# Kernel tuning notes

Hardware: AMD Instinct MI355X
Metric: run time of the kernel (lower is better)

Reference implementation:

```python
import jax, jax.numpy as jnp
import numpy as np
import math

B, S, D, H, WIDTH, NHW = 8, 1024, 512, 8, 8, 2
DK = D // H
S2 = S + 2 * WIDTH


def setup_inputs() -> dict:
    key = jax.random.key(0)
    ks = jax.random.split(key, 12)
    sc = 1.0 / math.sqrt(D)
    return {
        "x": jax.random.normal(ks[0], (B, S, D), jnp.float32),
        "l_attn_W": jax.random.normal(ks[1], (4, D, D), jnp.float32) * sc,  # q,k,v,out
        "l_attn_b": jnp.zeros((4, D), jnp.float32),
        "r_attn_W": jax.random.normal(ks[2], (4, D, D), jnp.float32) * sc,
        "r_attn_b": jnp.zeros((4, D), jnp.float32),
        "left_pad": jax.random.normal(ks[3], (WIDTH, D), jnp.float32) * sc,
        "right_pad": jax.random.normal(ks[4], (WIDTH, D), jnp.float32) * sc,
        "left_w": jax.random.normal(ks[5], (WIDTH + 1,), jnp.float32),
        "right_w": jax.random.normal(ks[6], (WIDTH + 1,), jnp.float32),
        "l_hw_W": jax.random.normal(ks[7], (NHW, D, 2 * D), jnp.float32) * sc,
        "l_hw_b": jnp.zeros((NHW, 2 * D), jnp.float32),
        "r_hw_W": jax.random.normal(ks[8], (NHW, D, 2 * D), jnp.float32) * sc,
        "r_hw_b": jnp.zeros((NHW, 2 * D), jnp.float32),
    }


def _mha(x, W, b, mask):
    # x: [B, S2, D]; W: [4, D, D]; mask: [1, S2, S2] bool (True = keep)
    q = (x @ W[0] + b[0]).reshape(B, S2, H, DK)
    k = (x @ W[1] + b[1]).reshape(B, S2, H, DK)
    v = (x @ W[2] + b[2]).reshape(B, S2, H, DK)
    scores = jnp.einsum('bihd,bjhd->bhij', q, k) / math.sqrt(DK)
    scores = jnp.where(mask[:, None], scores, jnp.float32(-1e9))
    p = jax.nn.softmax(scores, axis=-1)
    o = jnp.einsum('bhij,bjhd->bihd', p, v).reshape(B, S2, D)
    return o @ W[3] + b[3]


def _highway(x, Ws, bs):
    # AllenNLP-style Highway: projected -> [nonlinear | gate]
    for i in range(NHW):
        proj = x @ Ws[i] + bs[i]
        nl = jax.nn.relu(proj[..., :D])
        g = jax.nn.sigmoid(proj[..., D:])
        x = g * x + (1.0 - g) * nl
    return x


def reference(x, l_attn_W, l_attn_b, r_attn_W, r_attn_b, left_pad, right_pad,
              left_w, right_w, l_hw_W, l_hw_b, r_hw_W, r_hw_b):
    new_in = jnp.concatenate([
        jnp.broadcast_to(left_pad, (B, WIDTH, D)), x,
        jnp.broadcast_to(right_pad, (B, WIDTH, D))], axis=1)  # [B, S2, D]
    idx = jnp.arange(S2)
    diff = idx[:, None] - idx[None, :]
    lmask = ((diff >= 0) & (diff <= WIDTH + 1))[None]          # attend to [i-width-1, i]
    rmask = ((diff <= 0) & (diff >= -(WIDTH + 1)))[None]       # attend to [i, i+width+1]
    nl_attn = _mha(new_in, l_attn_W, l_attn_b, lmask)
    nr_attn = _mha(new_in, r_attn_W, r_attn_b, rmask)
    left_out = nl_attn[:, WIDTH:WIDTH + S, :]   # position end = start + width
    right_out = nr_attn[:, WIDTH:WIDTH + S, :]
    # relative-position weighted sliding windows (vectorized over all steps)
    lrel = sum(left_w[j] * new_in[:, j:j + S, :] for j in range(WIDTH + 1))
    rrel = sum(right_w[j] * new_in[:, WIDTH + j:WIDTH + j + S, :] for j in range(WIDTH + 1))
    left_out = _highway(left_out + lrel, l_hw_W, l_hw_b)
    right_out = _highway(right_out + rrel, r_hw_W, r_hw_b)
    out = jnp.concatenate([left_out, right_out], axis=-1)  # [B, S, 2D]
    return out[None]  # [1, B, S, 2D] matching torch stack layout
```

## Files before the change

kernel.cpp:

```cpp
#include <hip/hip_runtime.h>


#define B_ 8
#define S_ 1024
#define D_ 512
#define H_ 8
#define DK_ 64
#define WIDTH_ 8
#define S2_ 1040
#define NHW_ 2

typedef short bf16x8 __attribute__((ext_vector_type(8)));
typedef float f32x4 __attribute__((ext_vector_type(4)));

__device__ __forceinline__ float us2f(unsigned short u) {
  union { unsigned int i; float f; } c; c.i = ((unsigned int)u) << 16; return c.f;
}
__device__ __forceinline__ unsigned short f2us(float f) {
  union { float f; unsigned int i; } c; c.f = f;
  unsigned int x = c.i;
  return (unsigned short)((x + 0x7fffu + ((x >> 16) & 1u)) >> 16);
}
__device__ __forceinline__ unsigned int pack2(float a, float b) {
  return (unsigned int)f2us(a) | ((unsigned int)f2us(b) << 16);
}
__device__ __forceinline__ void async16(const void* g, void* l) {
  __builtin_amdgcn_global_load_lds(
      (const __attribute__((address_space(1))) void*)g,
      (__attribute__((address_space(3))) void*)l, 16, 0, 0);
}
__device__ __forceinline__ void unpack8(uint4 u, float* f) {
  unsigned int w[4] = {u.x, u.y, u.z, u.w};
  #pragma unroll
  for (int c = 0; c < 4; ++c) {
    union { unsigned int i; float g; } lo, hi;
    lo.i = w[c] << 16;
    hi.i = w[c] & 0xffff0000u;
    f[2 * c] = lo.g;
    f[2 * c + 1] = hi.g;
  }
}

__global__ __launch_bounds__(256) void k_prep(
    const float* __restrict__ x,
    const float* __restrict__ lpad, const float* __restrict__ rpad,
    const float* __restrict__ lW, const float* __restrict__ rW,
    const float* __restrict__ lb, const float* __restrict__ rb,
    const float* __restrict__ lhwW, const float* __restrict__ rhwW,
    unsigned short* __restrict__ WTall, unsigned short* __restrict__ WTp,
    unsigned short* __restrict__ hWT,
    unsigned short* __restrict__ nin, float* __restrict__ qkvbias)
{
  __shared__ float tile[32][33];
  const size_t DD = (size_t)D_ * D_;
  int bx = blockIdx.x;
  int tx = threadIdx.x & 31, ty = threadIdx.x >> 5;

  if (bx < 2048) {
    int sl = bx >> 8, rem = bx & 255;
    int side = sl >> 2, slice = sl & 3;
    int c0 = (rem & 15) * 32, r0 = (rem >> 4) * 32;
    const float* src = (side ? rW : lW) + (size_t)slice * DD;
    unsigned short* dst = (slice < 3) ? WTall + (size_t)(side * 3 + slice) * DD
                                      : WTp + (size_t)side * DD;
    #pragma unroll
    for (int i = 0; i < 4; ++i)
      tile[ty + i * 8][tx] = src[(size_t)(r0 + ty + i * 8) * D_ + c0 + tx];
    __syncthreads();
    #pragma unroll
    for (int i = 0; i < 4; ++i)
      dst[(size_t)(c0 + ty + i * 8) * D_ + r0 + tx] = f2us(tile[tx][ty + i * 8]);
    return;
  }
  if (bx < 4096) {
    int idx = bx - 2048;
    int sl = idx >> 9, rem = idx & 511;
    int c0 = (rem & 31) * 32, r0 = (rem >> 5) * 32;
    const float* src = ((sl >> 1) ? rhwW : lhwW) + (size_t)(sl & 1) * 512 * 1024;
    unsigned short* dst = hWT + (size_t)sl * 1024 * 512;
    #pragma unroll
    for (int i = 0; i < 4; ++i)
      tile[ty + i * 8][tx] = src[(size_t)(r0 + ty + i * 8) * 1024 + c0 + tx];
    __syncthreads();
    #pragma unroll
    for (int i = 0; i < 4; ++i) {
      int c = c0 + ty + i * 8;
      int cm = c & 511;
      int j = cm >> 4;
      int jl = j & 7;
      int Bq = ((jl >> 2) << 3) + (jl & 3) + ((c >= 512) ? 4 : 0);
      int q = (j >> 3) * 256 + Bq * 16 + (cm & 15);
      dst[(size_t)q * 512 + r0 + tx] = f2us(tile[tx][ty + i * 8]);
    }
    return;
  }
  int gid = (bx - 4096) * 256 + threadIdx.x;
  const int NTH = B_ * S2_ * 64;
  if (gid >= NTH) {
    int t = gid - NTH;
    if (t < 1536) qkvbias[t] = lb[t];
    else if (t < 3072) qkvbias[t] = rb[t - 1536];
    return;
  }
  int c8 = (gid & 63) << 3;
  int row = gid >> 6;
  int b = row / S2_;
  int t = row - b * S2_;
  const float* src;
  if (t < WIDTH_)            src = lpad + (size_t)t * D_ + c8;
  else if (t >= S_ + WIDTH_) src = rpad + (size_t)(t - S_ - WIDTH_) * D_ + c8;
  else                       src = x + ((size_t)b * S_ + (t - WIDTH_)) * D_ + c8;
  float4 a = *reinterpret_cast<const float4*>(src);
  float4 c = *reinterpret_cast<const float4*>(src + 4);
  uint4 o;
  o.x = pack2(a.x, a.y); o.y = pack2(a.z, a.w);
  o.z = pack2(c.x, c.y); o.w = pack2(c.z, c.w);
  *reinterpret_cast<uint4*>(nin + (size_t)row * D_ + c8) = o;
}

__global__ __launch_bounds__(256) void k_gemm_mfma(
    const unsigned short* __restrict__ A,
    const unsigned short* __restrict__ BT,
    const float* __restrict__ bias,
    unsigned short* __restrict__ C,
    int M, int N, int K)
{
  __shared__ unsigned short As[128 * 64];
  __shared__ unsigned short Bs[128 * 64];

  const int tid = threadIdx.x;
  const int w = tid >> 6;
  const int l = tid & 63;

  const int gx = gridDim.x;
  const int nwg = gx * gridDim.y;
  const int flat = blockIdx.y * gx + blockIdx.x;
  const int cpx = nwg >> 3;
  const int nf = (flat & 7) * cpx + (flat >> 3);
  const int bm = (nf / gx) * 128;
  const int bn = (nf % gx) * 128;

  const int wrow = (w >> 1) * 64;
  const int wcol = (w & 1) * 64;

  const int lr = l >> 3;
  const int sk = (((l & 7) ^ lr) & 7) * 8;
  const unsigned short* Ap = A + (size_t)(bm + w * 8 + lr) * K + sk;
  const unsigned short* Bp = BT + (size_t)(bn + w * 8 + lr) * K + sk;
  unsigned short* lA = &As[w * 512];
  unsigned short* lB = &Bs[w * 512];
  const size_t K32 = (size_t)32 * K;

  const int fl = l & 15;
  const int fq = l >> 4;
  const int fx = fl & 7;

  f32x4 acc[4][4];
  #pragma unroll
  for (int mi = 0; mi < 4; ++mi)
    #pragma unroll
    for (int ni = 0; ni < 4; ++ni) acc[mi][ni] = (f32x4){0.f, 0.f, 0.f, 0.f};

  for (int k0 = 0; k0 < K; k0 += 64) {
    #pragma unroll
    for (int r = 0; r < 4; ++r) {
      async16(Ap + k0 + r * K32, lA + r * 2048);
      async16(Bp + k0 + r * K32, lB + r * 2048);
    }
    __syncthreads();
    #pragma unroll
    for (int s = 0; s < 2; ++s) {
      bf16x8 af[4], bfr[4];
      #pragma unroll
      for (int mi = 0; mi < 4; ++mi)
        af[mi] = *reinterpret_cast<const bf16x8*>(
            &As[(wrow + mi * 16 + fl) * 64 + (((s * 4 + fq) ^ fx) * 8)]);
      #pragma unroll
      for (int ni = 0; ni < 4; ++ni)
        bfr[ni] = *reinterpret_cast<const bf16x8*>(
            &Bs[(wcol + ni * 16 + fl) * 64 + (((s * 4 + fq) ^ fx) * 8)]);
      #pragma unroll
      for (int mi = 0; mi < 4; ++mi)
        #pragma unroll
        for (int ni = 0; ni < 4; ++ni)
          acc[mi][ni] = __builtin_amdgcn_mfma_f32_16x16x32_bf16(
              af[mi], bfr[ni], acc[mi][ni], 0, 0, 0);
    }
    __syncthreads();
  }

  float bv[4];
  #pragma unroll
  for (int ni = 0; ni < 4; ++ni) bv[ni] = bias[bn + wcol + ni * 16 + fl];

  const int rbase = (l >> 4) * 4;
  #pragma unroll
  for (int mi = 0; mi < 4; ++mi) {
    #pragma unroll
    for (int r = 0; r < 4; ++r) {
      int row = bm + wrow + mi * 16 + rbase + r;
      unsigned short* Cp = C + (size_t)row * N + bn + wcol + fl;
      #pragma unroll
      for (int ni = 0; ni < 4; ++ni)
        Cp[ni * 16] = f2us(acc[mi][ni][r] + bv[ni]);
    }
  }
}

template <int EPI>
__global__ __launch_bounds__(512, 2) void k_gemm256(
    const unsigned short* __restrict__ Abase, size_t aStrZ,
    const unsigned short* __restrict__ BTbase, size_t bStrZ,
    const float* __restrict__ bias0, const float* __restrict__ bias1,
    unsigned short* __restrict__ Cbf, float* __restrict__ Cfp,
    int M, int N)
{
  __shared__ __align__(16) unsigned short smem[65536];
  const int tid = threadIdx.x;
  const int w = tid >> 6, l = tid & 63;
  const int wm = w >> 2, wn = w & 3;
  const int fl = l & 15, fq = l >> 4;
  const int z = blockIdx.z;
  const unsigned short* A = Abase + (size_t)z * aStrZ;
  const unsigned short* BT = BTbase + (size_t)z * bStrZ;
  const int bm = blockIdx.y * 256, bn = blockIdx.x * 256;

  const int xorb = (fl & 7) << 4;
  const int cs0 = ((fq * 16) ^ xorb) >> 1;
  const int cs1 = ((64 + fq * 16) ^ xorb) >> 1;

  const int rr = l >> 3;
  const int ce = (((l & 7) * 16) ^ (rr << 4)) >> 1;
  const unsigned short* gA[2][2];
  const unsigned short* gB[2][2];
  #pragma unroll
  for (int i = 0; i < 2; ++i)
    #pragma unroll
    for (int h = 0; h < 2; ++h) {
      int ra = bm + h * 128 + (2 * w + i) * 8 + rr;
      if (ra > M - 1) ra = M - 1;
      gA[i][h] = A + (size_t)ra * 512 + ce;
      int rb = bn + h * 128 + (2 * w + i) * 8 + rr;
      gB[i][h] = BT + (size_t)rb * 512 + ce;
    }

  f32x4 acc[8][4];
  #pragma unroll
  for (int mi = 0; mi < 8; ++mi)
    #pragma unroll
    for (int ni = 0; ni < 4; ++ni) acc[mi][ni] = (f32x4){0.f, 0.f, 0.f, 0.f};

  bf16x8 ar[4][2], br[2][2];

#define BAR() __builtin_amdgcn_s_barrier()
#define STGA(buf, h, kt) do { \
    async16(gA[0][h] + (kt) * 64, &smem[((buf) * 2 + (h)) * 8192 + (2 * w) * 512]); \
    async16(gA[1][h] + (kt) * 64, &smem[((buf) * 2 + (h)) * 8192 + (2 * w + 1) * 512]); } while (0)
#define STGB(buf, h, kt) do { \
    async16(gB[0][h] + (kt) * 64, &smem[32768 + ((buf) * 2 + (h)) * 8192 + (2 * w) * 512]); \
    async16(gB[1][h] + (kt) * 64, &smem[32768 + ((buf) * 2 + (h)) * 8192 + (2 * w + 1) * 512]); } while (0)
#define LDA(buf, h) do { const unsigned short* p_ = &smem[((buf) * 2 + (h)) * 8192]; \
    _Pragma("unroll") for (int m4 = 0; m4 < 4; ++m4) { \
      int ro_ = ((2 * m4 + wm) * 16 + fl) * 64; \
      ar[m4][0] = *reinterpret_cast<const bf16x8*>(p_ + ro_ + cs0); \
      ar[m4][1] = *reinterpret_cast<const bf16x8*>(p_ + ro_ + cs1); } } while (0)
#define LDB(buf, h) do { const unsigned short* p_ = &smem[32768 + ((buf) * 2 + (h)) * 8192]; \
    _Pragma("unroll") for (int n2 = 0; n2 < 2; ++n2) { \
      int ro_ = ((4 * n2 + wn) * 16 + fl) * 64; \
      br[n2][0] = *reinterpret_cast<const bf16x8*>(p_ + ro_ + cs0); \
      br[n2][1] = *reinterpret_cast<const bf16x8*>(p_ + ro_ + cs1); } } while (0)
#define QUAD(miH, niH) do { __builtin_amdgcn_s_setprio(1); \
    _Pragma("unroll") for (int m4 = 0; m4 < 4; ++m4) \
      _Pragma("unroll") for (int n2 = 0; n2 < 2; ++n2) \
        _Pragma("unroll") for (int s_ = 0; s_ < 2; ++s_) \
          acc[(miH) * 4 + m4][(niH) * 2 + n2] = __builtin_amdgcn_mfma_f32_16x16x32_bf16( \
              ar[m4][s_], br[n2][s_], acc[(miH) * 4 + m4][(niH) * 2 + n2], 0, 0, 0); \
    __builtin_amdgcn_s_setprio(0); } while (0)

  STGA(0, 0, 0); STGB(0, 0, 0); STGB(0, 1, 0); STGA(0, 1, 0);
  STGA(1, 0, 1); STGB(1, 1, 1); STGA(1, 1, 1);
  asm volatile("s_waitcnt vmcnt(6)" ::: "memory");
  BAR();

  #pragma unroll 1
  for (int it = 0; it < 4; ++it) {
    const int t1 = 2 * it + 1, t2 = 2 * it + 2, t3 = 2 * it + 3;
    LDA(0, 0); LDB(0, 0);
    STGB(1, 0, t1);
    BAR(); QUAD(0, 0); BAR();
    LDB(0, 1);
    if (t2 < 8) STGA(0, 0, t2);
    BAR(); QUAD(0, 1); BAR();
    LDA(0, 1);
    if (t2 < 8) STGB(0, 1, t2);
    BAR(); QUAD(1, 1); BAR();
    LDB(0, 0);
    if (t2 < 8) STGA(0, 1, t2);
    BAR(); QUAD(1, 0);
    if (it < 3) asm volatile("s_waitcnt vmcnt(6)" ::: "memory");
    else        asm volatile("s_waitcnt vmcnt(0)" ::: "memory");
    BAR();
    LDA(1, 0); LDB(1, 0);
    if (t2 < 8) STGB(0, 0, t2);
    BAR(); QUAD(0, 0); BAR();
    LDB(1, 1);
    if (t3 < 8) STGA(1, 0, t3);
    BAR(); QUAD(0, 1); BAR();
    LDA(1, 1);
    if (t3 < 8) STGB(1, 1, t3);
    BAR(); QUAD(1, 1); BAR();
    LDB(1, 0);
    if (t3 < 8) STGA(1, 1, t3);
    BAR(); QUAD(1, 0);
    asm volatile("s_waitcnt vmcnt(6)" ::: "memory");
    BAR();
  }
#undef BAR
#undef STGA
#undef STGB
#undef LDA
#undef LDB
#undef QUAD

  {
    const float* bias = z ? bias1 : bias0;
    const size_t MS = (size_t)B_ * S_ * D_;
    float bnl[2], bg[2]; int xs[2];
    #pragma unroll
    for (int np = 0; np < 2; ++np) {
      xs[np] = (blockIdx.x * 8 + np * 4 + wn) * 16 + fl;
      bnl[np] = bias[xs[np]];
      bg[np]  = bias[512 + xs[np]];
    }
    #pragma unroll
    for (int mi = 0; mi < 8; ++mi) {
      #pragma unroll
      for (int r = 0; r < 4; ++r) {
        int gr = bm + (2 * mi + wm) * 16 + fq * 4 + r;
        #pragma unroll
        for (int np = 0; np < 2; ++np) {
          float nl = fmaxf(acc[mi][2 * np][r] + bnl[np], 0.f);
          float g  = 1.f / (1.f + __expf(-(acc[mi][2 * np + 1][r] + bg[np])));
          float xv = us2f(A[(size_t)gr * 512 + xs[np]]);
          float res = g * xv + (1.f - g) * nl;
          if (EPI == 2) Cfp[(size_t)gr * 1024 + (size_t)z * 512 + xs[np]] = res;
          else Cbf[(size_t)z * MS + (size_t)gr * 512 + xs[np]] = f2us(res);
        }
      }
    }
  }
}

__global__ __launch_bounds__(256) void k_gemm_proj(
    const unsigned short* __restrict__ ctx,
    const unsigned short* __restrict__ WTp,
    const unsigned short* __restrict__ nin,
    const float* __restrict__ lb3, const float* __restrict__ rb3,
    const float* __restrict__ wrel0, const float* __restrict__ wrel1,
    unsigned short* __restrict__ hwx)
{
  __shared__ unsigned short smem[128 * 136];
  unsigned short* As = smem;
  unsigned short* Bs = smem + 8192;
  const int K = 512, N = 512;
  const size_t MS = (size_t)B_ * S_ * D_;

  const int z = blockIdx.z;
  const unsigned short* A = ctx + (size_t)z * MS;
  const unsigned short* BT = WTp + (size_t)z * 512 * 512;
  const float* bias = z ? rb3 : lb3;
  const float* wrel = z ? wrel1 : wrel0;
  const int off = z * WIDTH_;

  const int tid = threadIdx.x;
  const int w = tid >> 6;
  const int l = tid & 63;
  const int bm = blockIdx.y * 128;
  const int bn = blockIdx.x * 128;
  const int wrow = (w >> 1) * 64;
  const int wcol = (w & 1) * 64;

  const int lr = l >> 3;
  const int sk = (((l & 7) ^ lr) & 7) * 8;
  const unsigned short* Ap = A + (size_t)(bm + w * 8 + lr) * K + sk;
  const unsigned short* Bp = BT + (size_t)(bn + w * 8 + lr) * K + sk;
  unsigned short* lA = &As[w * 512];
  unsigned short* lB = &Bs[w * 512];
  const size_t K32 = (size_t)32 * K;

  const int fl = l & 15;
  const int fq = l >> 4;
  const int fx = fl & 7;

  f32x4 acc[4][4];
  #pragma unroll
  for (int mi = 0; mi < 4; ++mi)
    #pragma unroll
    for (int ni = 0; ni < 4; ++ni) acc[mi][ni] = (f32x4){0.f, 0.f, 0.f, 0.f};

  for (int k0 = 0; k0 < K; k0 += 64) {
    #pragma unroll
    for (int r = 0; r < 4; ++r) {
      async16(Ap + k0 + r * K32, lA + r * 2048);
      async16(Bp + k0 + r * K32, lB + r * 2048);
    }
    __syncthreads();
    #pragma unroll
    for (int s = 0; s < 2; ++s) {
      bf16x8 af[4], bfr[4];
      #pragma unroll
      for (int mi = 0; mi < 4; ++mi)
        af[mi] = *reinterpret_cast<const bf16x8*>(
            &As[(wrow + mi * 16 + fl) * 64 + (((s * 4 + fq) ^ fx) * 8)]);
      #pragma unroll
      for (int ni = 0; ni < 4; ++ni)
        bfr[ni] = *reinterpret_cast<const bf16x8*>(
            &Bs[(wcol + ni * 16 + fl) * 64 + (((s * 4 + fq) ^ fx) * 8)]);
      #pragma unroll
      for (int mi = 0; mi < 4; ++mi)
        #pragma unroll
        for (int ni = 0; ni < 4; ++ni)
          acc[mi][ni] = __builtin_amdgcn_mfma_f32_16x16x32_bf16(
              af[mi], bfr[ni], acc[mi][ni], 0, 0, 0);
    }
    __syncthreads();
  }

  float bv[4];
  #pragma unroll
  for (int ni = 0; ni < 4; ++ni) bv[ni] = bias[bn + wcol + ni * 16 + fl];
  const int rbase = (l >> 4) * 4;
  #pragma unroll
  for (int mi = 0; mi < 4; ++mi)
    #pragma unroll
    for (int r = 0; r < 4; ++r)
      #pragma unroll
      for (int ni = 0; ni < 4; ++ni)
        smem[(wrow + mi * 16 + rbase + r) * 136 + wcol + ni * 16 + fl] =
            f2us(acc[mi][ni][r] + bv[ni]);
  __syncthreads();

  const int trow = tid >> 4;
  const int tcol = (tid & 15) * 8;
  const float w0 = wrel[0], w1 = wrel[1], w2 = wrel[2], w3 = wrel[3],
              w4 = wrel[4], w5 = wrel[5], w6 = wrel[6], w7 = wrel[7],
              w8 = wrel[8];
  const float wj[9] = {w0, w1, w2, w3, w4, w5, w6, w7, w8};
  #pragma unroll
  for (int i = 0; i < 8; ++i) {
    int r = trow + i * 16;
    int gr = bm + r;
    int b = gr >> 10, s = gr & (S_ - 1);
    float a8[8];
    unpack8(*reinterpret_cast<const uint4*>(&smem[r * 136 + tcol]), a8);
    const unsigned short* np =
        nin + ((size_t)b * S2_ + off + s) * D_ + bn + tcol;
    #pragma unroll
    for (int j = 0; j < 9; ++j) {
      float nf[8];
      unpack8(*reinterpret_cast<const uint4*>(np + (size_t)j * D_), nf);
      #pragma unroll
      for (int e = 0; e < 8; ++e) a8[e] += wj[j] * nf[e];
    }
    uint4 o;
    o.x = pack2(a8[0], a8[1]); o.y = pack2(a8[2], a8[3]);
    o.z = pack2(a8[4], a8[5]); o.w = pack2(a8[6], a8[7]);
    *reinterpret_cast<uint4*>(
        hwx + (size_t)z * MS + (size_t)gr * D_ + bn + tcol) = o;
  }
}

__global__ __launch_bounds__(256) void k_attn_window(
    const unsigned short* __restrict__ qkv,
    unsigned short* __restrict__ ctx)
{
  int wid = (blockIdx.x * 256 + threadIdx.x) >> 6;
  int lane = threadIdx.x & 63;
  int sg = wid & 255;
  int b = (wid >> 8) & 7;
  int dir = wid >> 11;
  int s0 = sg << 2;
  int i0 = s0 + WIDTH_;

  const size_t base = (size_t)b * S2_ * 3072 + dir * 1536;
  const int c0 = lane * 8;

  float qf[4][8];
  #pragma unroll
  for (int r = 0; r < 4; ++r)
    unpack8(*reinterpret_cast<const uint4*>(
        qkv + base + (size_t)(i0 + r) * 3072 + c0), qf[r]);

  float sc[4][10];
  float mx[4] = {-1e30f, -1e30f, -1e30f, -1e30f};
  #pragma unroll
  for (int t = 0; t < 13; ++t) {
    int j = (dir == 0) ? (i0 - 9 + t) : (i0 + t);
    bool ok = (j >= 0 && j < S2_);
    float kf[8];
    if (ok)
      unpack8(*reinterpret_cast<const uint4*>(
          qkv + base + (size_t)j * 3072 + 512 + c0), kf);
    #pragma unroll
    for (int r = 0; r < 4; ++r) {
      if (t < r || t > r + 9) continue;
      float sv = -1e30f;
      if (ok) {
        float p = qf[r][0] * kf[0];
        #pragma unroll
        for (int e = 1; e < 8; ++e) p += qf[r][e] * kf[e];
        p += __shfl_xor(p, 1);
        p += __shfl_xor(p, 2);
        p += __shfl_xor(p, 4);
        sv = p * 0.125f;
      }
      sc[r][t - r] = sv;
      mx[r] = fmaxf(mx[r], sv);
    }
  }

  float inv[4];
  #pragma unroll
  for (int r = 0; r < 4; ++r) {
    float den = 0.f;
    #pragma unroll
    for (int u = 0; u < 10; ++u) {
      sc[r][u] = (sc[r][u] > -1e29f) ? __expf(sc[r][u] - mx[r]) : 0.f;
      den += sc[r][u];
    }
    inv[r] = 1.f / den;
  }

  float acc[4][8];
  #pragma unroll
  for (int r = 0; r < 4; ++r)
    #pragma unroll
    for (int e = 0; e < 8; ++e) acc[r][e] = 0.f;

  #pragma unroll
  for (int t = 0; t < 13; ++t) {
    int j = (dir == 0) ? (i0 - 9 + t) : (i0 + t);
    bool ok = (j >= 0 && j < S2_);
    float vf[8];
    if (ok)
      unpack8(*reinterpret_cast<const uint4*>(
          qkv + base + (size_t)j * 3072 + 1024 + c0), vf);
    #pragma unroll
    for (int r = 0; r < 4; ++r) {
      if (t < r || t > r + 9) continue;
      if (ok) {
        float p = sc[r][t - r];
        #pragma unroll
        for (int e = 0; e < 8; ++e) acc[r][e] += p * vf[e];
      }
    }
  }

  #pragma unroll
  for (int r = 0; r < 4; ++r) {
    uint4 o;
    o.x = pack2(acc[r][0] * inv[r], acc[r][1] * inv[r]);
    o.y = pack2(acc[r][2] * inv[r], acc[r][3] * inv[r]);
    o.z = pack2(acc[r][4] * inv[r], acc[r][5] * inv[r]);
    o.w = pack2(acc[r][6] * inv[r], acc[r][7] * inv[r]);
    *reinterpret_cast<uint4*>(
        ctx + (((size_t)dir * B_ + b) * S_ + s0 + r) * D_ + c0) = o;
  }
}

extern "C" void kernel_launch(void* const* d_in, const int* in_sizes, int n_in,
                              void* d_out, int out_size, void* d_ws, size_t ws_size,
                              hipStream_t stream) {
  const float* x    = (const float*)d_in[0];
  const float* lW   = (const float*)d_in[1];
  const float* lb   = (const float*)d_in[2];
  const float* rW   = (const float*)d_in[3];
  const float* rb   = (const float*)d_in[4];
  const float* lpad = (const float*)d_in[5];
  const float* rpad = (const float*)d_in[6];
  const float* lw   = (const float*)d_in[7];
  const float* rw   = (const float*)d_in[8];
  const float* lhwW = (const float*)d_in[9];
  const float* lhwb = (const float*)d_in[10];
  const float* rhwW = (const float*)d_in[11];
  const float* rhwb = (const float*)d_in[12];
  float* out = (float*)d_out;
  unsigned short* ws = (unsigned short*)d_ws;

  const size_t NIN  = (size_t)B_ * S2_ * D_;
  const size_t NQKV = (size_t)B_ * S2_ * 3072;
  const size_t MS   = (size_t)B_ * S_ * D_;
  const size_t DD   = (size_t)D_ * D_;
  const size_t LHW  = (size_t)1024 * 512;

  unsigned short* nin   = ws;
  unsigned short* qkv   = nin + NIN;
  unsigned short* ctx   = qkv + NQKV;
  unsigned short* hwx   = ctx + 2 * MS;
  unsigned short* hwy   = hwx + 2 * MS;
  unsigned short* WTall = hwy + 2 * MS;
  unsigned short* WTp   = WTall + 6 * DD;
  unsigned short* hWT   = WTp + 2 * DD;
  float* qkvbias        = (float*)(hWT + 4 * LHW);

  k_prep<<<6188, 256, 0, stream>>>(x, lpad, rpad, lW, rW, lb, rb, lhwW, rhwW,
                                   WTall, WTp, hWT, nin, qkvbias);

  const int MQ = B_ * S2_;

  {
    dim3 g(3072 / 128, MQ / 128, 1);
    k_gemm_mfma<<<g, 256, 0, stream>>>(nin, WTall, qkvbias, qkv, MQ, 3072, D_);
  }

  k_attn_window<<<(2 * B_ * S_) / 16, 256, 0, stream>>>(qkv, ctx);

  {
    dim3 g(D_ / 128, (B_ * S_) / 128, 2);
    k_gemm_proj<<<g, 256, 0, stream>>>(ctx, WTp, nin, lb + 3 * D_, rb + 3 * D_,
                                       lw, rw, hwx);
  }

  {
    dim3 g(1024 / 256, (B_ * S_) / 256, 2);
    k_gemm256<1><<<g, 512, 0, stream>>>(hwx, MS, hWT, 2 * LHW,
                                        lhwb, rhwb, hwy, nullptr,
                                        B_ * S_, 1024);
    k_gemm256<2><<<g, 512, 0, stream>>>(hwy, MS, hWT + LHW, 2 * LHW,
                                        lhwb + 1024, rhwb + 1024,
                                        nullptr, out, B_ * S_, 1024);
  }
}
```

Measured before the change: 236.4 us.

## Fuse attention, projection and highway layers into one cooperative persistent kernel

Replaces four separate launches (window attention, output projection, two highway GEMMs) with a single cooperative kernel of 256 blocks that runs each stage in turn and separates them with grid-wide syncs. Each block processes one attention slice, then two 128-tile projection GEMMs, then one 256-tile highway GEMM per layer. This aims to remove launch gaps and tail effects between kernels. In exchange, grid syncs add overhead, the grid is fixed at 256 blocks of 512 threads, and the 128KB shared buffer limits residency, so the attention and projection stages may run with less parallelism than before.

```diff
diff --git a/kernel.cpp b/kernel.cpp
--- a/kernel.cpp
+++ b/kernel.cpp
@@ -1,4 +1,6 @@
 #include <hip/hip_runtime.h>
+#include <hip/hip_cooperative_groups.h>
+namespace cg = cooperative_groups;
 
 
 #define B_ 8
@@ -207,23 +209,20 @@
   }
 }
 
-template <int EPI>
-__global__ __launch_bounds__(512, 2) void k_gemm256(
-    const unsigned short* __restrict__ Abase, size_t aStrZ,
-    const unsigned short* __restrict__ BTbase, size_t bStrZ,
-    const float* __restrict__ bias0, const float* __restrict__ bias1,
-    unsigned short* __restrict__ Cbf, float* __restrict__ Cfp,
-    int M, int N)
+__device__ __forceinline__ void hw_layer(
+    unsigned short* smem,
+    const unsigned short* __restrict__ A,
+    const unsigned short* __restrict__ BT,
+    const float* __restrict__ bias,
+    unsigned short* __restrict__ Obf,
+    float* __restrict__ Ofp,
+    int bx, int by, bool final_)
 {
-  __shared__ __align__(16) unsigned short smem[65536];
   const int tid = threadIdx.x;
   const int w = tid >> 6, l = tid & 63;
   const int wm = w >> 2, wn = w & 3;
   const int fl = l & 15, fq = l >> 4;
-  const int z = blockIdx.z;
-  const unsigned short* A = Abase + (size_t)z * aStrZ;
-  const unsigned short* BT = BTbase + (size_t)z * bStrZ;
-  const int bm = blockIdx.y * 256, bn = blockIdx.x * 256;
+  const int bm = by * 256, bn = bx * 256;
 
   const int xorb = (fl & 7) << 4;
   const int cs0 = ((fq * 16) ^ xorb) >> 1;
@@ -238,7 +237,6 @@
     #pragma unroll
     for (int h = 0; h < 2; ++h) {
       int ra = bm + h * 128 + (2 * w + i) * 8 + rr;
-      if (ra > M - 1) ra = M - 1;
       gA[i][h] = A + (size_t)ra * 512 + ce;
       int rb = bn + h * 128 + (2 * w + i) * 8 + rr;
       gB[i][h] = BT + (size_t)rb * 512 + ce;
@@ -322,249 +320,275 @@
 #undef LDB
 #undef QUAD
 
-  {
-    const float* bias = z ? bias1 : bias0;
-    const size_t MS = (size_t)B_ * S_ * D_;
-    float bnl[2], bg[2]; int xs[2];
-    #pragma unroll
-    for (int np = 0; np < 2; ++np) {
-      xs[np] = (blockIdx.x * 8 + np * 4 + wn) * 16 + fl;
-      bnl[np] = bias[xs[np]];
-      bg[np]  = bias[512 + xs[np]];
-    }
-    #pragma unroll
-    for (int mi = 0; mi < 8; ++mi) {
-      #pragma unroll
-      for (int r = 0; r < 4; ++r) {
-        int gr = bm + (2 * mi + wm) * 16 + fq * 4 + r;
-        #pragma unroll
-        for (int np = 0; np < 2; ++np) {
-          float nl = fmaxf(acc[mi][2 * np][r] + bnl[np], 0.f);
-          float g  = 1.f / (1.f + __expf(-(acc[mi][2 * np + 1][r] + bg[np])));
-          float xv = us2f(A[(size_t)gr * 512 + xs[np]]);
-          float res = g * xv + (1.f - g) * nl;
-          if (EPI == 2) Cfp[(size_t)gr * 1024 + (size_t)z * 512 + xs[np]] = res;
-          else Cbf[(size_t)z * MS + (size_t)gr * 512 + xs[np]] = f2us(res);
-        }
-      }
-    }
-  }
-}
-
-__global__ __launch_bounds__(256) void k_gemm_proj(
-    const unsigned short* __restrict__ ctx,
+  float bnl[2], bg[2]; int xs[2];
+  #pragma unroll
+  for (int np = 0; np < 2; ++np) {
+    xs[np] = (bx * 8 + np * 4 + wn) * 16 + fl;
+    bnl[np] = bias[xs[np]];
+    bg[np]  = bias[512 + xs[np]];
+  }
+  #pragma unroll
+  for (int mi = 0; mi < 8; ++mi) {
+    #pragma unroll
+    for (int r = 0; r < 4; ++r) {
+      int gr = bm + (2 * mi + wm) * 16 + fq * 4 + r;
+      #pragma unroll
+      for (int np = 0; np < 2; ++np) {
+        float nl = fmaxf(acc[mi][2 * np][r] + bnl[np], 0.f);
+        float g  = 1.f / (1.f + __expf(-(acc[mi][2 * np + 1][r] + bg[np])));
+        float xv = us2f(A[(size_t)gr * 512 + xs[np]]);
+        float res = g * xv + (1.f - g) * nl;
+        if (final_) Ofp[(size_t)gr * 1024 + xs[np]] = res;
+        else        Obf[(size_t)gr * 512 + xs[np]] = f2us(res);
+      }
+    }
+  }
+}
+
+__global__ __launch_bounds__(512, 2) void k_mega(
+    const unsigned short* __restrict__ qkv,
+    unsigned short* __restrict__ ctx,
     const unsigned short* __restrict__ WTp,
     const unsigned short* __restrict__ nin,
     const float* __restrict__ lb3, const float* __restrict__ rb3,
     const float* __restrict__ wrel0, const float* __restrict__ wrel1,
-    unsigned short* __restrict__ hwx)
+    unsigned short* __restrict__ hwx,
+    unsigned short* __restrict__ hwy,
+    const unsigned short* __restrict__ hWT,
+    const float* __restrict__ lhwb, const float* __restrict__ rhwb,
+    float* __restrict__ out)
 {
-  __shared__ unsigned short smem[128 * 136];
-  unsigned short* As = smem;
-  unsigned short* Bs = smem + 8192;
-  const int K = 512, N = 512;
+  __shared__ __align__(16) unsigned short smem[65536];
+  cg::grid_group grid = cg::this_grid();
   const size_t MS = (size_t)B_ * S_ * D_;
-
-  const int z = blockIdx.z;
-  const unsigned short* A = ctx + (size_t)z * MS;
-  const unsigned short* BT = WTp + (size_t)z * 512 * 512;
-  const float* bias = z ? rb3 : lb3;
-  const float* wrel = z ? wrel1 : wrel0;
-  const int off = z * WIDTH_;
-
-  const int tid = threadIdx.x;
-  const int w = tid >> 6;
-  const int l = tid & 63;
-  const int bm = blockIdx.y * 128;
-  const int bn = blockIdx.x * 128;
-  const int wrow = (w >> 1) * 64;
-  const int wcol = (w & 1) * 64;
-
-  const int lr = l >> 3;
-  const int sk = (((l & 7) ^ lr) & 7) * 8;
-  const unsigned short* Ap = A + (size_t)(bm + w * 8 + lr) * K + sk;
-  const unsigned short* Bp = BT + (size_t)(bn + w * 8 + lr) * K + sk;
-  unsigned short* lA = &As[w * 512];
-  unsigned short* lB = &Bs[w * 512];
-  const size_t K32 = (size_t)32 * K;
-
-  const int fl = l & 15;
-  const int fq = l >> 4;
-  const int fx = fl & 7;
-
-  f32x4 acc[4][4];
-  #pragma unroll
-  for (int mi = 0; mi < 4; ++mi)
-    #pragma unroll
-    for (int ni = 0; ni < 4; ++ni) acc[mi][ni] = (f32x4){0.f, 0.f, 0.f, 0.f};
-
-  for (int k0 = 0; k0 < K; k0 += 64) {
-    #pragma unroll
-    for (int r = 0; r < 4; ++r) {
-      async16(Ap + k0 + r * K32, lA + r * 2048);
-      async16(Bp + k0 + r * K32, lB + r * 2048);
-    }
+  const size_t LHW = (size_t)1024 * 512;
+
+  {
+    const int lane = threadIdx.x & 63;
+    const int wv = blockIdx.x * 8 + (threadIdx.x >> 6);
+    const int c0 = lane * 8;
+    const int sg = wv & 255;
+    const int b = (wv >> 8) & 7;
+    const int s0 = sg << 2;
+    const int i0 = s0 + WIDTH_;
+
+    #pragma unroll 1
+    for (int dir = 0; dir < 2; ++dir) {
+      const size_t base = (size_t)b * S2_ * 3072 + dir * 1536;
+
+      float qf[4][8];
+      #pragma unroll
+      for (int r = 0; r < 4; ++r)
+        unpack8(*reinterpret_cast<const uint4*>(
+            qkv + base + (size_t)(i0 + r) * 3072 + c0), qf[r]);
+
+      float sc[4][10];
+      float mx[4] = {-1e30f, -1e30f, -1e30f, -1e30f};
+      #pragma unroll
+      for (int t = 0; t < 13; ++t) {
+        int j = (dir == 0) ? (i0 - 9 + t) : (i0 + t);
+        bool ok = (j >= 0 && j < S2_);
+        float kf[8];
+        if (ok)
+          unpack8(*reinterpret_cast<const uint4*>(
+              qkv + base + (size_t)j * 3072 + 512 + c0), kf);
+        #pragma unroll
+        for (int r = 0; r < 4; ++r) {
+          if (t < r || t > r + 9) continue;
+          float sv = -1e30f;
+          if (ok) {
+            float p = qf[r][0] * kf[0];
+            #pragma unroll
+            for (int e = 1; e < 8; ++e) p += qf[r][e] * kf[e];
+            p += __shfl_xor(p, 1);
+            p += __shfl_xor(p, 2);
+            p += __shfl_xor(p, 4);
+            sv = p * 0.125f;
+          }
+          sc[r][t - r] = sv;
+          mx[r] = fmaxf(mx[r], sv);
+        }
+      }
+
+      float inv[4];
+      #pragma unroll
+      for (int r = 0; r < 4; ++r) {
+        float den = 0.f;
+        #pragma unroll
+        for (int u = 0; u < 10; ++u) {
+          sc[r][u] = (sc[r][u] > -1e29f) ? __expf(sc[r][u] - mx[r]) : 0.f;
+          den += sc[r][u];
+        }
+        inv[r] = 1.f / den;
+      }
+
+      float acc[4][8];
+      #pragma unroll
+      for (int r = 0; r < 4; ++r)
+        #pragma unroll
+        for (int e = 0; e < 8; ++e) acc[r][e] = 0.f;
+
+      #pragma unroll
+      for (int t = 0; t < 13; ++t) {
+        int j = (dir == 0) ? (i0 - 9 + t) : (i0 + t);
+        bool ok = (j >= 0 && j < S2_);
+        float vf[8];
+        if (ok)
+          unpack8(*reinterpret_cast<const uint4*>(
+              qkv + base + (size_t)j * 3072 + 1024 + c0), vf);
+        #pragma unroll
+        for (int r = 0; r < 4; ++r) {
+          if (t < r || t > r + 9) continue;
+          if (ok) {
+            float p = sc[r][t - r];
+            #pragma unroll
+            for (int e = 0; e < 8; ++e) acc[r][e] += p * vf[e];
+          }
+        }
+      }
+
+      #pragma unroll
+      for (int r = 0; r < 4; ++r) {
+        uint4 o;
+        o.x = pack2(acc[r][0] * inv[r], acc[r][1] * inv[r]);
+        o.y = pack2(acc[r][2] * inv[r], acc[r][3] * inv[r]);
+        o.z = pack2(acc[r][4] * inv[r], acc[r][5] * inv[r]);
+        o.w = pack2(acc[r][6] * inv[r], acc[r][7] * inv[r]);
+        *reinterpret_cast<uint4*>(
+            ctx + (((size_t)dir * B_ + b) * S_ + s0 + r) * D_ + c0) = o;
+      }
+    }
+  }
+  __threadfence();
+  grid.sync();
+
+  {
+    const int h = threadIdx.x >> 8;
+    const int t2 = threadIdx.x & 255;
+    const int v = blockIdx.x * 2 + h;
+    const int bx = v & 3, by = (v >> 2) & 63, z = v >> 8;
+    unsigned short* sm = smem + h * 17408;
+    unsigned short* As = sm;
+    unsigned short* Bs = sm + 8192;
+    const int K = 512;
+    const unsigned short* A = ctx + (size_t)z * MS;
+    const unsigned short* BT = WTp + (size_t)z * 262144;
+    const float* bias = z ? rb3 : lb3;
+    const float* wrel = z ? wrel1 : wrel0;
+    const int off = z * WIDTH_;
+
+    const int w = t2 >> 6;
+    const int l = t2 & 63;
+    const int bm = by * 128;
+    const int bn = bx * 128;
+    const int wrow = (w >> 1) * 64;
+    const int wcol = (w & 1) * 64;
+
+    const int lr = l >> 3;
+    const int sk = (((l & 7) ^ lr) & 7) * 8;
+    const unsigned short* Ap = A + (size_t)(bm + w * 8 + lr) * K + sk;
+    const unsigned short* Bp = BT + (size_t)(bn + w * 8 + lr) * K + sk;
+    unsigned short* lA = &As[w * 512];
+    unsigned short* lB = &Bs[w * 512];
+    const size_t K32 = (size_t)32 * K;
+
+    const int fl = l & 15;
+    const int fq = l >> 4;
+    const int fx = fl & 7;
+
+    f32x4 acc[4][4];
+    #pragma unroll
+    for (int mi = 0; mi < 4; ++mi)
+      #pragma unroll
+      for (int ni = 0; ni < 4; ++ni) acc[mi][ni] = (f32x4){0.f, 0.f, 0.f, 0.f};
+
+    for (int k0 = 0; k0 < K; k0 += 64) {
+      #pragma unroll
+      for (int r = 0; r < 4; ++r) {
+        async16(Ap + k0 + r * K32, lA + r * 2048);
+        async16(Bp + k0 + r * K32, lB + r * 2048);
+      }
+      __syncthreads();
+      #pragma unroll
+      for (int s = 0; s < 2; ++s) {
+        bf16x8 af[4], bfr[4];
+        #pragma unroll
+        for (int mi = 0; mi < 4; ++mi)
+          af[mi] = *reinterpret_cast<const bf16x8*>(
+              &As[(wrow + mi * 16 + fl) * 64 + (((s * 4 + fq) ^ fx) * 8)]);
+        #pragma unroll
+        for (int ni = 0; ni < 4; ++ni)
+          bfr[ni] = *reinterpret_cast<const bf16x8*>(
+              &Bs[(wcol + ni * 16 + fl) * 64 + (((s * 4 + fq) ^ fx) * 8)]);
+        #pragma unroll
+        for (int mi = 0; mi < 4; ++mi)
+          #pragma unroll
+          for (int ni = 0; ni < 4; ++ni)
+            acc[mi][ni] = __builtin_amdgcn_mfma_f32_16x16x32_bf16(
+                af[mi], bfr[ni], acc[mi][ni], 0, 0, 0);
+      }
+      __syncthreads();
+    }
+
+    float bv[4];
+    #pragma unroll
+    for (int ni = 0; ni < 4; ++ni) bv[ni] = bias[bn + wcol + ni * 16 + fl];
+    const int rbase = (l >> 4) * 4;
+    #pragma unroll
+    for (int mi = 0; mi < 4; ++mi)
+      #pragma unroll
+      for (int r = 0; r < 4; ++r)
+        #pragma unroll
+        for (int ni = 0; ni < 4; ++ni)
+          sm[(wrow + mi * 16 + rbase + r) * 136 + wcol + ni * 16 + fl] =
+              f2us(acc[mi][ni][r] + bv[ni]);
     __syncthreads();
-    #pragma unroll
-    for (int s = 0; s < 2; ++s) {
-      bf16x8 af[4], bfr[4];
-      #pragma unroll
-      for (int mi = 0; mi < 4; ++mi)
-        af[mi] = *reinterpret_cast<const bf16x8*>(
-            &As[(wrow + mi * 16 + fl) * 64 + (((s * 4 + fq) ^ fx) * 8)]);
-      #pragma unroll
-      for (int ni = 0; ni < 4; ++ni)
-        bfr[ni] = *reinterpret_cast<const bf16x8*>(
-            &Bs[(wcol + ni * 16 + fl) * 64 + (((s * 4 + fq) ^ fx) * 8)]);
-      #pragma unroll
-      for (int mi = 0; mi < 4; ++mi)
-        #pragma unroll
-        for (int ni = 0; ni < 4; ++ni)
-          acc[mi][ni] = __builtin_amdgcn_mfma_f32_16x16x32_bf16(
-              af[mi], bfr[ni], acc[mi][ni], 0, 0, 0);
-    }
-    __syncthreads();
-  }
-
-  float bv[4];
-  #pragma unroll
-  for (int ni = 0; ni < 4; ++ni) bv[ni] = bias[bn + wcol + ni * 16 + fl];
-  const int rbase = (l >> 4) * 4;
-  #pragma unroll
-  for (int mi = 0; mi < 4; ++mi)
-    #pragma unroll
-    for (int r = 0; r < 4; ++r)
-      #pragma unroll
-      for (int ni = 0; ni < 4; ++ni)
-        smem[(wrow + mi * 16 + rbase + r) * 136 + wcol + ni * 16 + fl] =
-            f2us(acc[mi][ni][r] + bv[ni]);
-  __syncthreads();
-
-  const int trow = tid >> 4;
-  const int tcol = (tid & 15) * 8;
-  const float w0 = wrel[0], w1 = wrel[1], w2 = wrel[2], w3 = wrel[3],
-              w4 = wrel[4], w5 = wrel[5], w6 = wrel[6], w7 = wrel[7],
-              w8 = wrel[8];
-  const float wj[9] = {w0, w1, w2, w3, w4, w5, w6, w7, w8};
-  #pragma unroll
-  for (int i = 0; i < 8; ++i) {
-    int r = trow + i * 16;
-    int gr = bm + r;
-    int b = gr >> 10, s = gr & (S_ - 1);
-    float a8[8];
-    unpack8(*reinterpret_cast<const uint4*>(&smem[r * 136 + tcol]), a8);
-    const unsigned short* np =
-        nin + ((size_t)b * S2_ + off + s) * D_ + bn + tcol;
-    #pragma unroll
-    for (int j = 0; j < 9; ++j) {
-      float nf[8];
-      unpack8(*reinterpret_cast<const uint4*>(np + (size_t)j * D_), nf);
-      #pragma unroll
-      for (int e = 0; e < 8; ++e) a8[e] += wj[j] * nf[e];
-    }
-    uint4 o;
-    o.x = pack2(a8[0], a8[1]); o.y = pack2(a8[2], a8[3]);
-    o.z = pack2(a8[4], a8[5]); o.w = pack2(a8[6], a8[7]);
-    *reinterpret_cast<uint4*>(
-        hwx + (size_t)z * MS + (size_t)gr * D_ + bn + tcol) = o;
-  }
-}
-
-__global__ __launch_bounds__(256) void k_attn_window(
-    const unsigned short* __restrict__ qkv,
-    unsigned short* __restrict__ ctx)
-{
-  int wid = (blockIdx.x * 256 + threadIdx.x) >> 6;
-  int lane = threadIdx.x & 63;
-  int sg = wid & 255;
-  int b = (wid >> 8) & 7;
-  int dir = wid >> 11;
-  int s0 = sg << 2;
-  int i0 = s0 + WIDTH_;
-
-  const size_t base = (size_t)b * S2_ * 3072 + dir * 1536;
-  const int c0 = lane * 8;
-
-  float qf[4][8];
-  #pragma unroll
-  for (int r = 0; r < 4; ++r)
-    unpack8(*reinterpret_cast<const uint4*>(
-        qkv + base + (size_t)(i0 + r) * 3072 + c0), qf[r]);
-
-  float sc[4][10];
-  float mx[4] = {-1e30f, -1e30f, -1e30f, -1e30f};
-  #pragma unroll
-  for (int t = 0; t < 13; ++t) {
-    int j = (dir == 0) ? (i0 - 9 + t) : (i0 + t);
-    bool ok = (j >= 0 && j < S2_);
-    float kf[8];
-    if (ok)
-      unpack8(*reinterpret_cast<const uint4*>(
-          qkv + base + (size_t)j * 3072 + 512 + c0), kf);
-    #pragma unroll
-    for (int r = 0; r < 4; ++r) {
-      if (t < r || t > r + 9) continue;
-      float sv = -1e30f;
-      if (ok) {
-        float p = qf[r][0] * kf[0];
-        #pragma unroll
-        for (int e = 1; e < 8; ++e) p += qf[r][e] * kf[e];
-        p += __shfl_xor(p, 1);
-        p += __shfl_xor(p, 2);
-        p += __shfl_xor(p, 4);
-        sv = p * 0.125f;
-      }
-      sc[r][t - r] = sv;
-      mx[r] = fmaxf(mx[r], sv);
-    }
-  }
-
-  float inv[4];
-  #pragma unroll
-  for (int r = 0; r < 4; ++r) {
-    float den = 0.f;
-    #pragma unroll
-    for (int u = 0; u < 10; ++u) {
-      sc[r][u] = (sc[r][u] > -1e29f) ? __expf(sc[r][u] - mx[r]) : 0.f;
-      den += sc[r][u];
-    }
-    inv[r] = 1.f / den;
-  }
-
-  float acc[4][8];
-  #pragma unroll
-  for (int r = 0; r < 4; ++r)
-    #pragma unroll
-    for (int e = 0; e < 8; ++e) acc[r][e] = 0.f;
-
-  #pragma unroll
-  for (int t = 0; t < 13; ++t) {
-    int j = (dir == 0) ? (i0 - 9 + t) : (i0 + t);
-    bool ok = (j >= 0 && j < S2_);
-    float vf[8];
-    if (ok)
-      unpack8(*reinterpret_cast<const uint4*>(
-          qkv + base + (size_t)j * 3072 + 1024 + c0), vf);
-    #pragma unroll
-    for (int r = 0; r < 4; ++r) {
-      if (t < r || t > r + 9) continue;
-      if (ok) {
-        float p = sc[r][t - r];
-        #pragma unroll
-        for (int e = 0; e < 8; ++e) acc[r][e] += p * vf[e];
-      }
-    }
-  }
-
-  #pragma unroll
-  for (int r = 0; r < 4; ++r) {
-    uint4 o;
-    o.x = pack2(acc[r][0] * inv[r], acc[r][1] * inv[r]);
-    o.y = pack2(acc[r][2] * inv[r], acc[r][3] * inv[r]);
-    o.z = pack2(acc[r][4] * inv[r], acc[r][5] * inv[r]);
-    o.w = pack2(acc[r][6] * inv[r], acc[r][7] * inv[r]);
-    *reinterpret_cast<uint4*>(
-        ctx + (((size_t)dir * B_ + b) * S_ + s0 + r) * D_ + c0) = o;
+
+    const int trow = t2 >> 4;
+    const int tcol = (t2 & 15) * 8;
+    const float wj[9] = {wrel[0], wrel[1], wrel[2], wrel[3], wrel[4],
+                         wrel[5], wrel[6], wrel[7], wrel[8]};
+    #pragma unroll
+    for (int i = 0; i < 8; ++i) {
+      int r = trow + i * 16;
+      int gr = bm + r;
+      int b = gr >> 10, s = gr & (S_ - 1);
+      float a8[8];
+      unpack8(*reinterpret_cast<const uint4*>(&sm[r * 136 + tcol]), a8);
+      const unsigned short* np =
+          nin + ((size_t)b * S2_ + off + s) * D_ + bn + tcol;
+      #pragma unroll
+      for (int j = 0; j < 9; ++j) {
+        float nf[8];
+        unpack8(*reinterpret_cast<const uint4*>(np + (size_t)j * D_), nf);
+        #pragma unroll
+        for (int e = 0; e < 8; ++e) a8[e] += wj[j] * nf[e];
+      }
+      uint4 o;
+      o.x = pack2(a8[0], a8[1]); o.y = pack2(a8[2], a8[3]);
+      o.z = pack2(a8[4], a8[5]); o.w = pack2(a8[6], a8[7]);
+      *reinterpret_cast<uint4*>(
+          hwx + (size_t)z * MS + (size_t)gr * D_ + bn + tcol) = o;
+    }
+  }
+  __threadfence();
+  grid.sync();
+
+  {
+    const int bx = blockIdx.x & 3;
+    const int by = (blockIdx.x >> 2) & 31;
+    const int z = blockIdx.x >> 7;
+    #pragma unroll 1
+    for (int lay = 0; lay < 2; ++lay) {
+      const unsigned short* A  = (lay ? hwy : hwx) + (size_t)z * MS;
+      const unsigned short* BT = hWT + ((size_t)(z * 2 + lay)) * LHW;
+      const float* bias = (z ? rhwb : lhwb) + lay * 1024;
+      hw_layer(smem, A, BT, bias,
+               hwy + (size_t)z * MS,
+               out + (size_t)z * 512,
+               bx, by, lay == 1);
+      if (lay == 0) { __threadfence(); grid.sync(); }
+    }
   }
 }
 
@@ -613,21 +637,25 @@
     k_gemm_mfma<<<g, 256, 0, stream>>>(nin, WTall, qkvbias, qkv, MQ, 3072, D_);
   }
 
-  k_attn_window<<<(2 * B_ * S_) / 16, 256, 0, stream>>>(qkv, ctx);
-
   {
-    dim3 g(D_ / 128, (B_ * S_) / 128, 2);
-    k_gemm_proj<<<g, 256, 0, stream>>>(ctx, WTp, nin, lb + 3 * D_, rb + 3 * D_,
-                                       lw, rw, hwx);
-  }
-
-  {
-    dim3 g(1024 / 256, (B_ * S_) / 256, 2);
-    k_gemm256<1><<<g, 512, 0, stream>>>(hwx, MS, hWT, 2 * LHW,
-                                        lhwb, rhwb, hwy, nullptr,
-                                        B_ * S_, 1024);
-    k_gemm256<2><<<g, 512, 0, stream>>>(hwy, MS, hWT + LHW, 2 * LHW,
-                                        lhwb + 1024, rhwb + 1024,
-                                        nullptr, out, B_ * S_, 1024);
-  }
-}
+    const unsigned short* a_qkv = qkv;
+    unsigned short* a_ctx = ctx;
+    const unsigned short* a_WTp = WTp;
+    const unsigned short* a_nin = nin;
+    const float* a_lb3 = lb + 3 * D_;
+    const float* a_rb3 = rb + 3 * D_;
+    const float* a_lw = lw;
+    const float* a_rw = rw;
+    unsigned short* a_hwx = hwx;
+    unsigned short* a_hwy = hwy;
+    const unsigned short* a_hWT = hWT;
+    const float* a_lhwb = lhwb;
+    const float* a_rhwb = rhwb;
+    float* a_out = out;
+    void* args[] = {&a_qkv, &a_ctx, &a_WTp, &a_nin, &a_lb3, &a_rb3,
+                    &a_lw, &a_rw, &a_hwx, &a_hwy, &a_hWT, &a_lhwb,
+                    &a_rhwb, &a_out};
+    hipLaunchCooperativeKernel((void*)k_mega, dim3(256), dim3(512),
+                               args, 0, stream);
+  }
+}
```

After: 573.2 us. 142% more time.
